# Optimization experiments

Hardware: AMD Instinct MI355X
Metric: run time of the kernel (lower is better)

The kernel has to match this reference:

```python
import jax, jax.numpy as jnp
import numpy as np
from jax import lax

B, C, H, W = 16, 256, 32, 32
HK, WK = 16, 16
NH = 8              # num_heads
HD = C // NH        # head_dim = 32
N = H * W           # 1024
M = HK * WK         # 256
EXP = 3             # attn_expansion
HID = NH * EXP      # 24 hidden channels in DLA
EPS = 1e-5


def setup_inputs() -> dict:
    key = jax.random.key(0)
    ks = jax.random.split(key, 16)
    s = 0.02
    return {
        "q": jax.random.normal(ks[0], (B, C, H, W), jnp.float32),
        "kv": jax.random.normal(ks[1], (B, C, HK, WK), jnp.float32),
        "Wq": jax.random.normal(ks[2], (C, C), jnp.float32) * s,
        "Wkv": jax.random.normal(ks[3], (2 * C, C), jnp.float32) * s,
        "Wp": jax.random.normal(ks[4], (C, C), jnp.float32) * s,
        "bp": jnp.zeros((C,), jnp.float32),
        "rpb": jnp.ones((N, M), jnp.float32),
        "W_exp": jax.random.normal(ks[5], (HID, NH), jnp.float32) * s,   # 1x1 conv heads->hidden
        "g1": jnp.ones((HID,), jnp.float32),
        "b1": jnp.zeros((HID,), jnp.float32),
        "W_dw": jax.random.normal(ks[6], (HID, 1, 3, 3), jnp.float32) * s,  # depthwise 3x3
        "g2": jnp.ones((HID,), jnp.float32),
        "b2": jnp.zeros((HID,), jnp.float32),
        "W_red": jax.random.normal(ks[7], (NH, HID), jnp.float32) * s,  # 1x1 conv hidden->heads
        "g3": jnp.ones((NH,), jnp.float32),
        "b3": jnp.zeros((NH,), jnp.float32),
    }


def group_norm(x, gamma, beta, groups):
    b, c, h, w = x.shape
    xg = x.reshape(b, groups, c // groups, h, w)
    mu = xg.mean(axis=(2, 3, 4), keepdims=True)
    var = xg.var(axis=(2, 3, 4), keepdims=True)
    xn = ((xg - mu) * lax.rsqrt(var + EPS)).reshape(b, c, h, w)
    return xn * gamma[None, :, None, None] + beta[None, :, None, None]


def swish(x):
    return x * jax.nn.sigmoid(x)


def dla(a, W_exp, g1, b1, W_dw, g2, b2, W_red, g3, b3):
    # a: [B, NH, N, M] treated as NCHW image with C=num_heads
    x = jnp.einsum('bcnm,oc->bonm', a, W_exp)              # 1x1 expand -> [B,HID,N,M]
    x = swish(group_norm(x, g1, b1, EXP))
    x = lax.conv_general_dilated(
        x, W_dw, window_strides=(1, 1), padding='SAME',
        feature_group_count=HID,
        dimension_numbers=('NCHW', 'OIHW', 'NCHW'))        # depthwise 3x3
    x = swish(group_norm(x, g2, b2, EXP))
    x = jnp.einsum('bcnm,oc->bonm', x, W_red)              # 1x1 reduce -> [B,NH,N,M]
    x = group_norm(x, g3, b3, 1)                            # no activation
    return x


def reference(q, kv, Wq, Wkv, Wp, bp, rpb, W_exp, g1, b1, W_dw, g2, b2, W_red, g3, b3):
    b = q.shape[0]
    scale = HD ** -0.5
    # kv path: [B,C,HK,WK] -> [B,M,C] -> Linear(C->2C)
    kv_t = kv.reshape(b, C, M).transpose(0, 2, 1)
    kvp = kv_t @ Wkv.T                                     # [B,M,2C]
    kvp = kvp.reshape(b, M, 2, NH, HD).transpose(2, 0, 3, 1, 4)  # [2,B,NH,M,HD]
    k, v = kvp[0], kvp[1]
    # q path: [B,C,H,W] -> [B,N,C] -> Linear -> [B,NH,N,HD]
    qf = (q.reshape(b, C, N).transpose(0, 2, 1) @ Wq.T)
    qh = qf.reshape(b, N, NH, HD).transpose(0, 2, 1, 3)
    attn = jnp.einsum('bhnd,bhmd->bhnm', qh, k) * scale + rpb[None, None]
    attn = jax.nn.softmax(attn, axis=-1)
    attn = dla(attn, W_exp, g1, b1, W_dw, g2, b2, W_red, g3, b3)
    out = jnp.einsum('bhnm,bhmd->bhnd', attn, v)           # [B,NH,N,HD]
    out = out.transpose(0, 2, 1, 3).reshape(b, N, C)
    out = out @ Wp.T + bp
    return out.transpose(0, 2, 1).reshape(b, C, H, W)
```

## Files before the change

### kernel.cpp

```cpp
#include <hip/hip_runtime.h>
#include <math.h>

#define Bb 16
#define Cc 256
#define Nn 1024
#define Mm 256
#define NHh 8
#define HDd 32
#define HIDh 24
#define NMs (Nn*Mm)
#define TTB 16
#define CHUNK 8
#define EPSf 1e-5f
#define SCALEf 0.17677669529663687f
#define STP 32

typedef float v2f __attribute__((ext_vector_type(2)));
typedef __attribute__((ext_vector_type(8))) short bf8v;
typedef __attribute__((ext_vector_type(4))) float f4v;

__device__ __forceinline__ float wave_sum(float v){
#pragma unroll
  for (int off=32; off; off>>=1) v += __shfl_xor(v, off, 64);
  return v;
}
__device__ __forceinline__ float sigm_(float x){ return __builtin_amdgcn_rcpf(1.f + __expf(-x)); }
__device__ __forceinline__ float swish_(float x){ return x * sigm_(x); }
__device__ __forceinline__ v2f swish2(v2f x){
  v2f r;
  r.x = x.x * sigm_(x.x);
  r.y = x.y * sigm_(x.y);
  return r;
}
__device__ __forceinline__ unsigned short f2bf(float f){
  unsigned u = __float_as_uint(f);
  u += 0x7fffu + ((u >> 16) & 1u);
  return (unsigned short)(u >> 16);
}
__device__ __forceinline__ unsigned cvtpk(float lo, float hi){
  unsigned r;
  asm("v_cvt_pk_bf16_f32 %0, %1, %2" : "=v"(r) : "v"(lo), "v"(hi));
  return r;
}
__device__ __forceinline__ float bfup(unsigned short s){ return __uint_as_float(((unsigned)s) << 16); }
__device__ __forceinline__ float bflo(unsigned u){ return __uint_as_float(u << 16); }
__device__ __forceinline__ float bfhi(unsigned u){ return __uint_as_float(u & 0xffff0000u); }
__device__ __forceinline__ void gload_lds16(const void* g, void* l){
  __builtin_amdgcn_global_load_lds(
      (const __attribute__((address_space(1))) unsigned int*)g,
      (__attribute__((address_space(3))) unsigned int*)l, 16, 0, 0);
}

template<int MODE>
__launch_bounds__(256)
__global__ void gemm_mfma(const float* __restrict__ A,
                          const float* __restrict__ W,
                          const float* __restrict__ bias,
                          float* __restrict__ O1, float* __restrict__ O2, int Isize)
{
  __shared__ __align__(16) unsigned short Wt[64 * 40];
  __shared__ __align__(16) unsigned short At[64 * 40];
  const int b = blockIdx.z;
  const int i0 = blockIdx.x * 64;
  const int j0 = blockIdx.y * 64;
  const int tid = threadIdx.x;
  const int lane = tid & 63, wv = tid >> 6;
  const int wj = (wv >> 1) * 32, wi = (wv & 1) * 32;
  const int l15 = lane & 15, l4 = lane >> 4;

  const float* Ab = A + (long)b * Cc * Isize;
  const int sj = tid >> 2, skh = (tid & 3) * 8;
  const int si = tid & 63, skb = (tid >> 6) * 8;

  f4v acc[2][2] = {};
  for (int k0 = 0; k0 < Cc; k0 += 32) {
    float wreg[8];
    {
      const float* wp = W + (long)(j0 + sj) * Cc + k0 + skh;
      *(f4v*)&wreg[0] = *(const f4v*)&wp[0];
      *(f4v*)&wreg[4] = *(const f4v*)&wp[4];
    }
    float areg[8];
    {
      const float* ap = Ab + (long)(k0 + skb) * Isize + i0 + si;
#pragma unroll
      for (int e = 0; e < 8; e++) areg[e] = ap[(long)e * Isize];
    }
    __syncthreads();
    {
      unsigned pk[4];
#pragma unroll
      for (int t = 0; t < 4; t++) pk[t] = cvtpk(wreg[2*t], wreg[2*t+1]);
      *(uint4*)&Wt[sj*40 + skh] = make_uint4(pk[0], pk[1], pk[2], pk[3]);
#pragma unroll
      for (int t = 0; t < 4; t++) pk[t] = cvtpk(areg[2*t], areg[2*t+1]);
      *(uint4*)&At[si*40 + skb] = make_uint4(pk[0], pk[1], pk[2], pk[3]);
    }
    __syncthreads();
    bf8v af[2], bf[2];
#pragma unroll
    for (int fm = 0; fm < 2; fm++)
      af[fm] = *(const bf8v*)&Wt[(wj + fm*16 + l15)*40 + l4*8];
#pragma unroll
    for (int fn = 0; fn < 2; fn++)
      bf[fn] = *(const bf8v*)&At[(wi + fn*16 + l15)*40 + l4*8];
#pragma unroll
    for (int fm = 0; fm < 2; fm++)
#pragma unroll
      for (int fn = 0; fn < 2; fn++)
        acc[fm][fn] = __builtin_amdgcn_mfma_f32_16x16x32_bf16(af[fm], bf[fn], acc[fm][fn], 0, 0, 0);
  }
#pragma unroll
  for (int fm = 0; fm < 2; fm++) {
    const int jb = j0 + wj + fm*16 + l4*4;
    f4v bv = {0.f, 0.f, 0.f, 0.f};
    if (MODE == 2) bv = *(const f4v*)&bias[jb];
#pragma unroll
    for (int fn = 0; fn < 2; fn++) {
      const int ii = i0 + wi + fn*16 + l15;
      if (MODE == 1) {
        const int two = jb >> 8, jj = jb & 255;
        const int h = jj >> 5, d0 = jj & 31;
        float* p = (two ? O2 : O1) + (((long)b * NHh + h) * Mm + ii) * HDd + d0;
#pragma unroll
        for (int r = 0; r < 4; r++) p[r] = acc[fm][fn][r];
      } else {
        float* op = O1 + ((long)b * Cc + jb) * (long)Isize + ii;
#pragma unroll
        for (int r = 0; r < 4; r++)
          op[(long)r * Isize] = acc[fm][fn][r] + bv[r];
      }
    }
  }
}

__launch_bounds__(256)
__global__ void compute_sv(const float* __restrict__ vb, float* __restrict__ sv)
{
  __shared__ float red[256];
  const int bh = blockIdx.x, tid = threadIdx.x;
  const int d = tid & 31, ch = tid >> 5;
  const float* vp = vb + (long)bh * Mm * HDd;
  float s = 0.f;
  for (int m = ch; m < Mm; m += 8) s += vp[m * HDd + d];
  red[tid] = s;
  __syncthreads();
  if (tid < 32) {
    float t = 0.f;
#pragma unroll
    for (int cc = 0; cc < 8; cc++) t += red[cc * 32 + tid];
    sv[(long)bh * HDd + tid] = t;
  }
}

__launch_bounds__(256)
__global__ void attn_softmax(const float* __restrict__ qhT, const float* __restrict__ kb,
                             const float* __restrict__ rpb, unsigned short* __restrict__ attn)
{
  __shared__ __align__(16) unsigned short Kt[Mm * 40];
  __shared__ __align__(16) unsigned short Qt[64 * 40];
  const int b = blockIdx.z, h = blockIdx.y, n0 = blockIdx.x * 64;
  const int tid = threadIdx.x;
  const int lane = tid & 63, wv = tid >> 6;
  const int l15 = lane & 15, l4 = lane >> 4;
  {
    const float* kp = kb + ((long)b * NHh + h) * Mm * HDd;
#pragma unroll
    for (int u = 0; u < 8; u++) {
      const int f = tid + u * 256;
      const int m = f >> 3, dq = (f & 7) * 4;
      const f4v k4 = *(const f4v*)&kp[m * HDd + dq];
      *(uint2*)&Kt[m * 40 + dq] = make_uint2(cvtpk(k4.x, k4.y), cvtpk(k4.z, k4.w));
    }
  }
  {
    const float* qp = qhT + ((long)b * NHh + h) * HDd * Nn + n0;
#pragma unroll
    for (int u = 0; u < 4; u++) {
      const int f = tid + u * 256;
      const int n = f & 63, d2 = (f >> 6) * 2;
      const float q0 = qp[(long)d2 * Nn + n];
      const float q1 = qp[(long)(d2 + 1) * Nn + n];
      *(unsigned*)&Qt[n * 40 + d2] = cvtpk(q0, q1);
    }
  }
  __syncthreads();
  const bf8v qf = *(const bf8v*)&Qt[(wv * 16 + l15) * 40 + l4 * 8];
  f4v S[16];
#pragma unroll
  for (int mt = 0; mt < 16; mt++) {
    const bf8v kf = *(const bf8v*)&Kt[(mt * 16 + l15) * 40 + l4 * 8];
    f4v z = {0.f, 0.f, 0.f, 0.f};
    S[mt] = __builtin_amdgcn_mfma_f32_16x16x32_bf16(kf, qf, z, 0, 0, 0);
  }
  const int n = n0 + wv * 16 + l15;
  const float* rp = rpb + (long)n * Mm;
  float mx = -1e30f;
#pragma unroll
  for (int mt = 0; mt < 16; mt++) {
    const f4v r4 = *(const f4v*)&rp[mt * 16 + l4 * 4];
    S[mt][0] = fmaf(S[mt][0], SCALEf, r4.x);
    S[mt][1] = fmaf(S[mt][1], SCALEf, r4.y);
    S[mt][2] = fmaf(S[mt][2], SCALEf, r4.z);
    S[mt][3] = fmaf(S[mt][3], SCALEf, r4.w);
    mx = fmaxf(mx, fmaxf(fmaxf(S[mt][0], S[mt][1]), fmaxf(S[mt][2], S[mt][3])));
  }
  mx = fmaxf(mx, __shfl_xor(mx, 16, 64));
  mx = fmaxf(mx, __shfl_xor(mx, 32, 64));
  float sum = 0.f;
#pragma unroll
  for (int mt = 0; mt < 16; mt++) {
    S[mt][0] = __expf(S[mt][0] - mx);
    S[mt][1] = __expf(S[mt][1] - mx);
    S[mt][2] = __expf(S[mt][2] - mx);
    S[mt][3] = __expf(S[mt][3] - mx);
    sum += (S[mt][0] + S[mt][1]) + (S[mt][2] + S[mt][3]);
  }
  sum += __shfl_xor(sum, 16, 64);
  sum += __shfl_xor(sum, 32, 64);
  const float inv = __builtin_amdgcn_rcpf(sum);
  unsigned short* ap = attn + (((long)b * NHh + h) * Nn + n) * Mm;
#pragma unroll
  for (int mt = 0; mt < 16; mt++) {
    const unsigned p0 = cvtpk(S[mt][0] * inv, S[mt][1] * inv);
    const unsigned p1 = cvtpk(S[mt][2] * inv, S[mt][3] * inv);
    *(uint2*)&ap[mt * 16 + l4 * 4] = make_uint2(p0, p1);
  }
}

__launch_bounds__(256)
__global__ void gram_stats(const unsigned short* __restrict__ attn, float* __restrict__ G)
{
  __shared__ float red[36][4];
  const int b = blockIdx.y, tid = threadIdx.x;
  const unsigned short* ap = attn + (long)b * NHh * NMs + (long)blockIdx.x * 2048 + tid * 8;
  float a[8][8];
#pragma unroll
  for (int h = 0; h < 8; h++) {
    const uint4 v = *(const uint4*)&ap[(long)h * NMs];
    a[h][0] = bflo(v.x); a[h][1] = bfhi(v.x); a[h][2] = bflo(v.y); a[h][3] = bfhi(v.y);
    a[h][4] = bflo(v.z); a[h][5] = bfhi(v.z); a[h][6] = bflo(v.w); a[h][7] = bfhi(v.w);
  }
  float g[36];
  int t = 0;
#pragma unroll
  for (int i = 0; i < 8; i++)
#pragma unroll
    for (int j = i; j < 8; j++, t++) {
      float s = 0.f;
#pragma unroll
      for (int m = 0; m < 8; m++) s = fmaf(a[i][m], a[j][m], s);
      g[t] = s;
    }
  const int lane = tid & 63, wid = tid >> 6;
#pragma unroll
  for (int t2 = 0; t2 < 36; t2++) {
    const float s = wave_sum(g[t2]);
    if (lane == 0) red[t2][wid] = s;
  }
  __syncthreads();
  if (tid < 36)
    atomicAdd(&G[((long)b * 36 + tid) * STP],
              red[tid][0] + red[tid][1] + red[tid][2] + red[tid][3]);
}

__launch_bounds__(768, 6)
__global__ void dla_pass_b(const unsigned short* __restrict__ attn,
                           const float* __restrict__ Wexp,
                           const float* __restrict__ g1, const float* __restrict__ b1,
                           const float* __restrict__ G, const float* __restrict__ Wdw,
                           unsigned short* __restrict__ x2, float* __restrict__ stats2c, int b0)
{
  __shared__ __align__(16) unsigned short sl[(TTB + 2) * NHh * Mm];
  const int tid = threadIdx.x;
  const int wv = tid >> 6, lane = tid & 63;
  const int bc = blockIdx.y, b = b0 + bc;
  const int n0 = blockIdx.x * TTB;
  const int c0 = wv * 2;
  const int g = wv >> 2;

  {
    const unsigned short* abase = attn + (long)b * NHh * NMs;
    const int q_lo = lane >> 5;
    const int m0 = (lane & 31) * 8;
#pragma unroll
    for (int i = 0; i < 6; i++) {
      const int pp = (wv * 6 + i) * 2;
      const int row = pp >> 3;
      const int nn = n0 - 1 + row;
      if (nn >= 0 && nn < Nn) {
        const int h = (pp + q_lo) & 7;
        gload_lds16(abase + (long)h * NMs + (long)nn * Mm + m0, &sl[pp * Mm]);
      }
    }
  }

  float mu, rs;
  {
    const float* Gb = G + (long)b * 36 * STP;
    float sum = 0.f, sumsq = 0.f;
    for (int c = g * 8; c < g * 8 + 8; c++) {
      float w[8];
#pragma unroll
      for (int h = 0; h < 8; h++) w[h] = Wexp[c * 8 + h];
      float wsu = 0.f;
#pragma unroll
      for (int h = 0; h < 8; h++) wsu += w[h];
      sum += wsu;
      float s2 = 0.f;
      int t = 0;
#pragma unroll
      for (int i = 0; i < 8; i++)
#pragma unroll
        for (int j = i; j < 8; j++, t++) {
          const float f = (i == j) ? 1.f : 2.f;
          s2 = fmaf(f * w[i] * w[j], Gb[t * STP], s2);
        }
      sumsq += s2;
    }
    const float cnt = 8.f * NMs;
    mu = sum * ((float)Nn / cnt);
    const float var = sumsq / cnt - mu * mu;
    rs = rsqrtf(var + EPSf);
  }
  v2f we2[8], wd2[9], B12;
  {
    const float A10 = rs * g1[c0], A11 = rs * g1[c0 + 1];
    B12.x = b1[c0] - mu * A10;
    B12.y = b1[c0 + 1] - mu * A11;
#pragma unroll
    for (int h = 0; h < NHh; h++) {
      we2[h].x = Wexp[c0 * NHh + h] * A10;
      we2[h].y = Wexp[(c0 + 1) * NHh + h] * A11;
    }
#pragma unroll
    for (int k = 0; k < 9; k++) {
      wd2[k].x = Wdw[c0 * 9 + k];
      wd2[k].y = Wdw[(c0 + 1) * 9 + k];
    }
  }
  __syncthreads();

  v2f s1p[4] = {}, s2p[4] = {};
  v2f smp = {0.f, 0.f}, sqp = {0.f, 0.f};
  for (int r = -1; r <= TTB; r++) {
    const int nn = n0 + r;
    const bool rowv = (nn >= 0 && nn < Nn);
    v2f xp[4];
    if (rowv) {
#pragma unroll
      for (int mi = 0; mi < 4; mi++) xp[mi] = B12;
      const unsigned short* sp = &sl[(r + 1) * NHh * Mm + lane * 4];
#pragma unroll
      for (int h = 0; h < NHh; h++) {
        const ushort4 v = *(const ushort4*)&sp[h * Mm];
        xp[0] += we2[h] * bfup(v.x);
        xp[1] += we2[h] * bfup(v.y);
        xp[2] += we2[h] * bfup(v.z);
        xp[3] += we2[h] * bfup(v.w);
      }
#pragma unroll
      for (int mi = 0; mi < 4; mi++) xp[mi] = swish2(xp[mi]);
    } else {
#pragma unroll
      for (int mi = 0; mi < 4; mi++) xp[mi] = (v2f){0.f, 0.f};
    }
    v2f xl, xr;
    xl.x = __shfl_up(xp[3].x, 1);  xl.y = __shfl_up(xp[3].y, 1);
    xr.x = __shfl_down(xp[0].x, 1); xr.y = __shfl_down(xp[0].y, 1);
    if (lane == 0)  { xl = (v2f){0.f, 0.f}; }
    if (lane == 63) { xr = (v2f){0.f, 0.f}; }
    const v2f L[4] = {xl, xp[0], xp[1], xp[2]};
    const v2f R[4] = {xp[1], xp[2], xp[3], xr};
    v2f y[4];
#pragma unroll
    for (int mi = 0; mi < 4; mi++) {
      const v2f u0 = wd2[0] * L[mi] + wd2[1] * xp[mi] + wd2[2] * R[mi];
      const v2f u1 = wd2[3] * L[mi] + wd2[4] * xp[mi] + wd2[5] * R[mi];
      const v2f u2 = wd2[6] * L[mi] + wd2[7] * xp[mi] + wd2[8] * R[mi];
      y[mi] = s2p[mi] + u2;
      s2p[mi] = s1p[mi] + u1;
      s1p[mi] = u0;
    }
    if (r >= 1) {
#pragma unroll
      for (int mi = 0; mi < 4; mi++) {
        smp += y[mi];
        sqp += y[mi] * y[mi];
      }
      const int nw = n0 + r - 1;
      const unsigned w0 = cvtpk(y[0].x, y[1].x), w1 = cvtpk(y[2].x, y[3].x);
      const unsigned w2 = cvtpk(y[0].y, y[1].y), w3 = cvtpk(y[2].y, y[3].y);
      unsigned short* xq = x2 + ((long)(bc * Nn + nw) * HIDh + c0) * Mm + lane * 4;
      *(uint2*)xq        = make_uint2(w0, w1);
      *(uint2*)(xq + Mm) = make_uint2(w2, w3);
    }
  }
  {
    const float vs0 = wave_sum(smp.x), vq0 = wave_sum(sqp.x);
    const float vs1 = wave_sum(smp.y), vq1 = wave_sum(sqp.y);
    if (lane == 0) {
      atomicAdd(&stats2c[((long)b * HIDh + c0) * STP], vs0);
      atomicAdd(&stats2c[((long)b * HIDh + c0) * STP + 1], vq0);
      atomicAdd(&stats2c[((long)b * HIDh + c0 + 1) * STP], vs1);
      atomicAdd(&stats2c[((long)b * HIDh + c0 + 1) * STP + 1], vq1);
    }
  }
}

__launch_bounds__(256)
__global__ void dla_pass_c(const unsigned short* __restrict__ x2, const float* __restrict__ g2,
                           const float* __restrict__ b2, const float* __restrict__ stats2c,
                           const float* __restrict__ Wred, unsigned short* __restrict__ a2,
                           float* __restrict__ partial3, int b0)
{
  __shared__ float wA[HIDh], wB[HIDh], wrs[HIDh][NHh];
  __shared__ float red2[2][4];
  const int tid = threadIdx.x;
  const int wv = tid >> 6, lane = tid & 63;
  const int bc = blockIdx.y, b = b0 + bc;
  if (tid < HIDh) {
    const int c = tid, g = c >> 3;
    float s = 0.f, q = 0.f;
#pragma unroll
    for (int cc = 0; cc < 8; cc++) {
      s += stats2c[((long)b * HIDh + g * 8 + cc) * STP];
      q += stats2c[((long)b * HIDh + g * 8 + cc) * STP + 1];
    }
    const float cnt = 8.f * NMs;
    const float mu = s / cnt;
    const float var = q / cnt - mu * mu;
    const float A2 = rsqrtf(var + EPSf) * g2[c];
    wA[c] = A2; wB[c] = b2[c] - mu * A2;
  }
  if (tid < HIDh * NHh) {
    const int c = tid >> 3, h = tid & 7;
    wrs[c][h] = Wred[h * HIDh + c];
  }
  __syncthreads();
  const int rsel = lane >> 5, ms = lane & 31;
  const int n = blockIdx.x * 8 + wv * 2 + rsel;
  const unsigned short* xp = x2 + (long)(bc * Nn + n) * HIDh * Mm + ms * 8;
  float red[NHh][8] = {};
#pragma unroll
  for (int c = 0; c < HIDh; c++) {
    const uint4 xv = *(const uint4*)&xp[c * Mm];
    const float Ac = wA[c], Bc = wB[c];
    float sw[8];
    sw[0] = swish_(fmaf(bflo(xv.x), Ac, Bc));
    sw[1] = swish_(fmaf(bfhi(xv.x), Ac, Bc));
    sw[2] = swish_(fmaf(bflo(xv.y), Ac, Bc));
    sw[3] = swish_(fmaf(bfhi(xv.y), Ac, Bc));
    sw[4] = swish_(fmaf(bflo(xv.z), Ac, Bc));
    sw[5] = swish_(fmaf(bfhi(xv.z), Ac, Bc));
    sw[6] = swish_(fmaf(bflo(xv.w), Ac, Bc));
    sw[7] = swish_(fmaf(bfhi(xv.w), Ac, Bc));
#pragma unroll
    for (int h = 0; h < NHh; h++) {
      const float w = wrs[c][h];
#pragma unroll
      for (int mi = 0; mi < 8; mi++) red[h][mi] = fmaf(w, sw[mi], red[h][mi]);
    }
  }
  float s3 = 0.f, q3 = 0.f;
#pragma unroll
  for (int h = 0; h < NHh; h++) {
    uint4 st;
    st.x = cvtpk(red[h][0], red[h][1]);
    st.y = cvtpk(red[h][2], red[h][3]);
    st.z = cvtpk(red[h][4], red[h][5]);
    st.w = cvtpk(red[h][6], red[h][7]);
    *(uint4*)&a2[(((long)b * NHh + h) * Nn + n) * Mm + ms * 8] = st;
#pragma unroll
    for (int mi = 0; mi < 8; mi++) {
      s3 += red[h][mi]; q3 = fmaf(red[h][mi], red[h][mi], q3);
    }
  }
  s3 = wave_sum(s3); q3 = wave_sum(q3);
  if (lane == 0) { red2[0][wv] = s3; red2[1][wv] = q3; }
  __syncthreads();
  if (tid < 2) {
    float t = red2[tid][0] + red2[tid][1] + red2[tid][2] + red2[tid][3];
    partial3[((long)b * 128 + blockIdx.x) * 2 + tid] = t;
  }
}

__launch_bounds__(128)
__global__ void finalize_stats3(const float* __restrict__ partial3, float* __restrict__ stats3)
{
  __shared__ float red2[2][2];
  const int b = blockIdx.x, tid = threadIdx.x;
  const int lane = tid & 63, wv = tid >> 6;
  float s = partial3[((long)b * 128 + tid) * 2];
  float q = partial3[((long)b * 128 + tid) * 2 + 1];
  s = wave_sum(s); q = wave_sum(q);
  if (lane == 0) { red2[0][wv] = s; red2[1][wv] = q; }
  __syncthreads();
  if (tid < 2)
    stats3[b * 2 + tid] = red2[tid][0] + red2[tid][1];
}

__launch_bounds__(256)
__global__ void pv_mfma(const unsigned short* __restrict__ a2, const float* __restrict__ vb,
                        const float* __restrict__ sv, const float* __restrict__ stats3,
                        const float* __restrict__ g3, const float* __restrict__ b3,
                        float* __restrict__ o)
{
  __shared__ __align__(16) unsigned short Vt[32 * 264];
  const int b = blockIdx.z, h = blockIdx.y, n0 = blockIdx.x * 128;
  const int tid = threadIdx.x;
  const int lane = tid & 63, wv = tid >> 6;
  const int l15 = lane & 15, l4 = lane >> 4;
  {
    const float* vp = vb + ((long)b * NHh + h) * Mm * HDd;
#pragma unroll
    for (int u = 0; u < 32; u++) {
      const int idx = tid + u * 256;
      const int m = idx >> 5, d = idx & 31;
      Vt[d * 264 + m] = f2bf(vp[idx]);
    }
  }
  __syncthreads();
  const unsigned short* ap = a2 + (((long)b * NHh + h) * Nn + n0) * Mm;
  f4v acc[2][2] = {};
#pragma unroll 2
  for (int k0 = 0; k0 < Mm; k0 += 32) {
    bf8v af[2], bf[2];
#pragma unroll
    for (int fm = 0; fm < 2; fm++)
      af[fm] = *(const bf8v*)&Vt[(fm * 16 + l15) * 264 + k0 + l4 * 8];
#pragma unroll
    for (int fn = 0; fn < 2; fn++)
      bf[fn] = *(const bf8v*)&ap[(long)(wv * 32 + fn * 16 + l15) * Mm + k0 + l4 * 8];
#pragma unroll
    for (int fm = 0; fm < 2; fm++)
#pragma unroll
      for (int fn = 0; fn < 2; fn++)
        acc[fm][fn] = __builtin_amdgcn_mfma_f32_16x16x32_bf16(af[fm], bf[fn], acc[fm][fn], 0, 0, 0);
  }
  const float cnt = (float)(NHh * NMs);
  const float mu = stats3[b * 2] / cnt;
  const float var = stats3[b * 2 + 1] / cnt - mu * mu;
  const float r3 = rsqrtf(var + EPSf);
  const float alpha = r3 * g3[h];
  const float beta = b3[h] - mu * alpha;
#pragma unroll
  for (int fm = 0; fm < 2; fm++) {
#pragma unroll
    for (int r = 0; r < 4; r++) {
      const int d = fm * 16 + l4 * 4 + r;
      const float bv = beta * sv[((long)b * NHh + h) * HDd + d];
      float* op = o + ((long)b * Cc + h * HDd + d) * Nn + n0 + wv * 32 + l15;
#pragma unroll
      for (int fn = 0; fn < 2; fn++)
        op[fn * 16] = fmaf(alpha, acc[fm][fn][r], bv);
    }
  }
}

extern "C" void kernel_launch(void* const* d_in, const int* in_sizes, int n_in,
                              void* d_out, int out_size, void* d_ws, size_t ws_size,
                              hipStream_t stream) {
  const float* q    = (const float*)d_in[0];
  const float* kv   = (const float*)d_in[1];
  const float* Wq   = (const float*)d_in[2];
  const float* Wkv  = (const float*)d_in[3];
  const float* Wp   = (const float*)d_in[4];
  const float* bp   = (const float*)d_in[5];
  const float* rpb  = (const float*)d_in[6];
  const float* Wexp = (const float*)d_in[7];
  const float* g1   = (const float*)d_in[8];
  const float* b1   = (const float*)d_in[9];
  const float* Wdw  = (const float*)d_in[10];
  const float* g2   = (const float*)d_in[11];
  const float* b2   = (const float*)d_in[12];
  const float* Wred = (const float*)d_in[13];
  const float* g3   = (const float*)d_in[14];
  const float* b3   = (const float*)d_in[15];
  float* out = (float*)d_out;

  float* ws = (float*)d_ws;
  size_t off = 0;
  auto alloc = [&](size_t n) { float* p = ws + off; off += n; return p; };
  float* attnf   = alloc((size_t)Bb * NHh * NMs / 2);
  float* a2f     = alloc((size_t)Bb * NHh * NMs / 2);
  float* big     = alloc((size_t)CHUNK * HIDh * NMs / 2);
  float* kbuf    = alloc((size_t)Bb * NHh * Mm * HDd);
  float* vbuf    = alloc((size_t)Bb * NHh * Mm * HDd);
  float* sv      = alloc((size_t)Bb * NHh * HDd);
  float* G       = alloc((size_t)Bb * 36 * STP);
  float* stats2c = alloc((size_t)Bb * HIDh * STP);
  float* stats3  = alloc(Bb * 2);
  float* partial3= alloc((size_t)Bb * 128 * 2);
  unsigned short* attn = (unsigned short*)attnf;
  unsigned short* a2 = (unsigned short*)a2f;
  float* qhT = big;
  unsigned short* x2 = (unsigned short*)big;
  float* oT = big;

  hipMemsetAsync(G, 0, (size_t)(Bb * 36 * STP + Bb * HIDh * STP) * sizeof(float), stream);

  gemm_mfma<0><<<dim3(Nn / 64, Cc / 64, Bb), 256, 0, stream>>>(q, Wq, nullptr, qhT, nullptr, Nn);
  gemm_mfma<1><<<dim3(Mm / 64, 512 / 64, Bb), 256, 0, stream>>>(kv, Wkv, nullptr, kbuf, vbuf, Mm);
  compute_sv<<<dim3(Bb * NHh), 256, 0, stream>>>(vbuf, sv);
  attn_softmax<<<dim3(Nn / 64, NHh, Bb), 256, 0, stream>>>(qhT, kbuf, rpb, attn);
  gram_stats<<<dim3(NMs / 2048, Bb), 256, 0, stream>>>(attn, G);

  for (int b0 = 0; b0 < Bb; b0 += CHUNK) {
    dla_pass_b<<<dim3(Nn / TTB, CHUNK), 768, 0, stream>>>(
        attn, Wexp, g1, b1, G, Wdw, x2, stats2c, b0);
    dla_pass_c<<<dim3(Nn / 8, CHUNK), 256, 0, stream>>>(
        x2, g2, b2, stats2c, Wred, a2, partial3, b0);
  }
  finalize_stats3<<<dim3(Bb), 128, 0, stream>>>(partial3, stats3);

  pv_mfma<<<dim3(Nn / 128, NHh, Bb), 256, 0, stream>>>(a2, vbuf, sv, stats3, g3, b3, oT);
  gemm_mfma<2><<<dim3(Nn / 64, Cc / 64, Bb), 256, 0, stream>>>(oT, Wp, bp, out, nullptr, Nn);
}
```

Baseline: 394.2 us.

## Store K/V as bf16, fuse sv and stats3 finalize into pv, pack dla_pass_c math

```diff
diff --git a/kernel.cpp b/kernel.cpp
--- a/kernel.cpp
+++ b/kernel.cpp
@@ -121,9 +121,10 @@
       if (MODE == 1) {
         const int two = jb >> 8, jj = jb & 255;
         const int h = jj >> 5, d0 = jj & 31;
-        float* p = (two ? O2 : O1) + (((long)b * NHh + h) * Mm + ii) * HDd + d0;
-#pragma unroll
-        for (int r = 0; r < 4; r++) p[r] = acc[fm][fn][r];
+        unsigned short* p = (unsigned short*)(two ? O2 : O1)
+                          + (((long)b * NHh + h) * Mm + ii) * HDd + d0;
+        *(uint2*)p = make_uint2(cvtpk(acc[fm][fn][0], acc[fm][fn][1]),
+                                cvtpk(acc[fm][fn][2], acc[fm][fn][3]));
       } else {
         float* op = O1 + ((long)b * Cc + jb) * (long)Isize + ii;
 #pragma unroll
@@ -135,26 +136,7 @@
 }
 
 __launch_bounds__(256)
-__global__ void compute_sv(const float* __restrict__ vb, float* __restrict__ sv)
-{
-  __shared__ float red[256];
-  const int bh = blockIdx.x, tid = threadIdx.x;
-  const int d = tid & 31, ch = tid >> 5;
-  const float* vp = vb + (long)bh * Mm * HDd;
-  float s = 0.f;
-  for (int m = ch; m < Mm; m += 8) s += vp[m * HDd + d];
-  red[tid] = s;
-  __syncthreads();
-  if (tid < 32) {
-    float t = 0.f;
-#pragma unroll
-    for (int cc = 0; cc < 8; cc++) t += red[cc * 32 + tid];
-    sv[(long)bh * HDd + tid] = t;
-  }
-}
-
-__launch_bounds__(256)
-__global__ void attn_softmax(const float* __restrict__ qhT, const float* __restrict__ kb,
+__global__ void attn_softmax(const float* __restrict__ qhT, const unsigned short* __restrict__ kb,
                              const float* __restrict__ rpb, unsigned short* __restrict__ attn)
 {
   __shared__ __align__(16) unsigned short Kt[Mm * 40];
@@ -164,13 +146,12 @@
   const int lane = tid & 63, wv = tid >> 6;
   const int l15 = lane & 15, l4 = lane >> 4;
   {
-    const float* kp = kb + ((long)b * NHh + h) * Mm * HDd;
-#pragma unroll
-    for (int u = 0; u < 8; u++) {
+    const unsigned short* kp = kb + ((long)b * NHh + h) * Mm * HDd;
+#pragma unroll
+    for (int u = 0; u < 4; u++) {
       const int f = tid + u * 256;
-      const int m = f >> 3, dq = (f & 7) * 4;
-      const f4v k4 = *(const f4v*)&kp[m * HDd + dq];
-      *(uint2*)&Kt[m * 40 + dq] = make_uint2(cvtpk(k4.x, k4.y), cvtpk(k4.z, k4.w));
+      const int m = f >> 2, q8 = (f & 3) * 8;
+      *(uint4*)&Kt[m * 40 + q8] = *(const uint4*)&kp[m * HDd + q8];
     }
   }
   {
@@ -415,7 +396,7 @@
                            float* __restrict__ partial3, int b0)
 {
   __shared__ float wA[HIDh], wB[HIDh], wrs[HIDh][NHh];
-  __shared__ float red2[2][4];
+  __shared__ float red2s[2][4];
   const int tid = threadIdx.x;
   const int wv = tid >> 6, lane = tid & 63;
   const int bc = blockIdx.y, b = b0 + bc;
@@ -441,86 +422,105 @@
   const int rsel = lane >> 5, ms = lane & 31;
   const int n = blockIdx.x * 8 + wv * 2 + rsel;
   const unsigned short* xp = x2 + (long)(bc * Nn + n) * HIDh * Mm + ms * 8;
-  float red[NHh][8] = {};
+  v2f red[NHh][4] = {};
 #pragma unroll
   for (int c = 0; c < HIDh; c++) {
     const uint4 xv = *(const uint4*)&xp[c * Mm];
-    const float Ac = wA[c], Bc = wB[c];
-    float sw[8];
-    sw[0] = swish_(fmaf(bflo(xv.x), Ac, Bc));
-    sw[1] = swish_(fmaf(bfhi(xv.x), Ac, Bc));
-    sw[2] = swish_(fmaf(bflo(xv.y), Ac, Bc));
-    sw[3] = swish_(fmaf(bfhi(xv.y), Ac, Bc));
-    sw[4] = swish_(fmaf(bflo(xv.z), Ac, Bc));
-    sw[5] = swish_(fmaf(bfhi(xv.z), Ac, Bc));
-    sw[6] = swish_(fmaf(bflo(xv.w), Ac, Bc));
-    sw[7] = swish_(fmaf(bfhi(xv.w), Ac, Bc));
+    const v2f A2 = {wA[c], wA[c]}, B2 = {wB[c], wB[c]};
+    v2f xw[4];
+    xw[0] = (v2f){bflo(xv.x), bfhi(xv.x)};
+    xw[1] = (v2f){bflo(xv.y), bfhi(xv.y)};
+    xw[2] = (v2f){bflo(xv.z), bfhi(xv.z)};
+    xw[3] = (v2f){bflo(xv.w), bfhi(xv.w)};
+#pragma unroll
+    for (int mi = 0; mi < 4; mi++) xw[mi] = swish2(xw[mi] * A2 + B2);
 #pragma unroll
     for (int h = 0; h < NHh; h++) {
       const float w = wrs[c][h];
-#pragma unroll
-      for (int mi = 0; mi < 8; mi++) red[h][mi] = fmaf(w, sw[mi], red[h][mi]);
-    }
-  }
-  float s3 = 0.f, q3 = 0.f;
+      const v2f w2 = {w, w};
+#pragma unroll
+      for (int mi = 0; mi < 4; mi++) red[h][mi] += w2 * xw[mi];
+    }
+  }
+  v2f s3v = {0.f, 0.f}, q3v = {0.f, 0.f};
 #pragma unroll
   for (int h = 0; h < NHh; h++) {
     uint4 st;
-    st.x = cvtpk(red[h][0], red[h][1]);
-    st.y = cvtpk(red[h][2], red[h][3]);
-    st.z = cvtpk(red[h][4], red[h][5]);
-    st.w = cvtpk(red[h][6], red[h][7]);
+    st.x = cvtpk(red[h][0].x, red[h][0].y);
+    st.y = cvtpk(red[h][1].x, red[h][1].y);
+    st.z = cvtpk(red[h][2].x, red[h][2].y);
+    st.w = cvtpk(red[h][3].x, red[h][3].y);
     *(uint4*)&a2[(((long)b * NHh + h) * Nn + n) * Mm + ms * 8] = st;
 #pragma unroll
-    for (int mi = 0; mi < 8; mi++) {
-      s3 += red[h][mi]; q3 = fmaf(red[h][mi], red[h][mi], q3);
-    }
-  }
+    for (int mi = 0; mi < 4; mi++) {
+      s3v += red[h][mi];
+      q3v += red[h][mi] * red[h][mi];
+    }
+  }
+  float s3 = s3v.x + s3v.y, q3 = q3v.x + q3v.y;
   s3 = wave_sum(s3); q3 = wave_sum(q3);
-  if (lane == 0) { red2[0][wv] = s3; red2[1][wv] = q3; }
+  if (lane == 0) { red2s[0][wv] = s3; red2s[1][wv] = q3; }
   __syncthreads();
   if (tid < 2) {
-    float t = red2[tid][0] + red2[tid][1] + red2[tid][2] + red2[tid][3];
+    float t = red2s[tid][0] + red2s[tid][1] + red2s[tid][2] + red2s[tid][3];
     partial3[((long)b * 128 + blockIdx.x) * 2 + tid] = t;
   }
 }
 
-__launch_bounds__(128)
-__global__ void finalize_stats3(const float* __restrict__ partial3, float* __restrict__ stats3)
-{
-  __shared__ float red2[2][2];
-  const int b = blockIdx.x, tid = threadIdx.x;
-  const int lane = tid & 63, wv = tid >> 6;
-  float s = partial3[((long)b * 128 + tid) * 2];
-  float q = partial3[((long)b * 128 + tid) * 2 + 1];
-  s = wave_sum(s); q = wave_sum(q);
-  if (lane == 0) { red2[0][wv] = s; red2[1][wv] = q; }
-  __syncthreads();
-  if (tid < 2)
-    stats3[b * 2 + tid] = red2[tid][0] + red2[tid][1];
-}
-
 __launch_bounds__(256)
-__global__ void pv_mfma(const unsigned short* __restrict__ a2, const float* __restrict__ vb,
-                        const float* __restrict__ sv, const float* __restrict__ stats3,
+__global__ void pv_mfma(const unsigned short* __restrict__ a2, const unsigned short* __restrict__ vb,
+                        const float* __restrict__ partial3,
                         const float* __restrict__ g3, const float* __restrict__ b3,
                         float* __restrict__ o)
 {
   __shared__ __align__(16) unsigned short Vt[32 * 264];
+  __shared__ float svl[32][9];
+  __shared__ float r4s[4];
   const int b = blockIdx.z, h = blockIdx.y, n0 = blockIdx.x * 128;
   const int tid = threadIdx.x;
   const int lane = tid & 63, wv = tid >> 6;
   const int l15 = lane & 15, l4 = lane >> 4;
   {
-    const float* vp = vb + ((long)b * NHh + h) * Mm * HDd;
+    const unsigned short* vp = vb + ((long)b * NHh + h) * Mm * HDd;
 #pragma unroll
     for (int u = 0; u < 32; u++) {
       const int idx = tid + u * 256;
       const int m = idx >> 5, d = idx & 31;
-      Vt[d * 264 + m] = f2bf(vp[idx]);
-    }
-  }
-  __syncthreads();
+      Vt[d * 264 + m] = vp[idx];
+    }
+  }
+  float pv_;
+  {
+    const int half = tid >> 7, i = tid & 127;
+    pv_ = partial3[((long)b * 128 + i) * 2 + half];
+  }
+  __syncthreads();
+  {
+    const int d = tid & 31, seg = tid >> 5;
+    float s = 0.f;
+#pragma unroll
+    for (int mm = 0; mm < 32; mm++) s += bfup(Vt[d * 264 + seg * 32 + mm]);
+    svl[d][seg] = s;
+  }
+  {
+    const float w = wave_sum(pv_);
+    if (lane == 0) r4s[wv] = w;
+  }
+  __syncthreads();
+  if (tid < 32) {
+    float t = 0.f;
+#pragma unroll
+    for (int seg = 0; seg < 8; seg++) t += svl[tid][seg];
+    svl[tid][0] = t;
+  }
+  __syncthreads();
+  const float cnt = (float)(NHh * NMs);
+  const float mu = (r4s[0] + r4s[1]) / cnt;
+  const float var = (r4s[2] + r4s[3]) / cnt - mu * mu;
+  const float r3 = rsqrtf(var + EPSf);
+  const float alpha = r3 * g3[h];
+  const float beta = b3[h] - mu * alpha;
+
   const unsigned short* ap = a2 + (((long)b * NHh + h) * Nn + n0) * Mm;
   f4v acc[2][2] = {};
 #pragma unroll 2
@@ -538,18 +538,12 @@
       for (int fn = 0; fn < 2; fn++)
         acc[fm][fn] = __builtin_amdgcn_mfma_f32_16x16x32_bf16(af[fm], bf[fn], acc[fm][fn], 0, 0, 0);
   }
-  const float cnt = (float)(NHh * NMs);
-  const float mu = stats3[b * 2] / cnt;
-  const float var = stats3[b * 2 + 1] / cnt - mu * mu;
-  const float r3 = rsqrtf(var + EPSf);
-  const float alpha = r3 * g3[h];
-  const float beta = b3[h] - mu * alpha;
 #pragma unroll
   for (int fm = 0; fm < 2; fm++) {
 #pragma unroll
     for (int r = 0; r < 4; r++) {
       const int d = fm * 16 + l4 * 4 + r;
-      const float bv = beta * sv[((long)b * NHh + h) * HDd + d];
+      const float bv = beta * svl[d][0];
       float* op = o + ((long)b * Cc + h * HDd + d) * Nn + n0 + wv * 32 + l15;
 #pragma unroll
       for (int fn = 0; fn < 2; fn++)
@@ -587,13 +581,13 @@
   float* big     = alloc((size_t)CHUNK * HIDh * NMs / 2);
   float* kbuf    = alloc((size_t)Bb * NHh * Mm * HDd);
   float* vbuf    = alloc((size_t)Bb * NHh * Mm * HDd);
-  float* sv      = alloc((size_t)Bb * NHh * HDd);
   float* G       = alloc((size_t)Bb * 36 * STP);
   float* stats2c = alloc((size_t)Bb * HIDh * STP);
-  float* stats3  = alloc(Bb * 2);
   float* partial3= alloc((size_t)Bb * 128 * 2);
   unsigned short* attn = (unsigned short*)attnf;
   unsigned short* a2 = (unsigned short*)a2f;
+  unsigned short* kb16 = (unsigned short*)kbuf;
+  unsigned short* vb16 = (unsigned short*)vbuf;
   float* qhT = big;
   unsigned short* x2 = (unsigned short*)big;
   float* oT = big;
@@ -602,8 +596,7 @@
 
   gemm_mfma<0><<<dim3(Nn / 64, Cc / 64, Bb), 256, 0, stream>>>(q, Wq, nullptr, qhT, nullptr, Nn);
   gemm_mfma<1><<<dim3(Mm / 64, 512 / 64, Bb), 256, 0, stream>>>(kv, Wkv, nullptr, kbuf, vbuf, Mm);
-  compute_sv<<<dim3(Bb * NHh), 256, 0, stream>>>(vbuf, sv);
-  attn_softmax<<<dim3(Nn / 64, NHh, Bb), 256, 0, stream>>>(qhT, kbuf, rpb, attn);
+  attn_softmax<<<dim3(Nn / 64, NHh, Bb), 256, 0, stream>>>(qhT, kb16, rpb, attn);
   gram_stats<<<dim3(NMs / 2048, Bb), 256, 0, stream>>>(attn, G);
 
   for (int b0 = 0; b0 < Bb; b0 += CHUNK) {
@@ -612,8 +605,7 @@
     dla_pass_c<<<dim3(Nn / 8, CHUNK), 256, 0, stream>>>(
         x2, g2, b2, stats2c, Wred, a2, partial3, b0);
   }
-  finalize_stats3<<<dim3(Bb), 128, 0, stream>>>(partial3, stats3);
-
-  pv_mfma<<<dim3(Nn / 128, NHh, Bb), 256, 0, stream>>>(a2, vbuf, sv, stats3, g3, b3, oT);
+
+  pv_mfma<<<dim3(Nn / 128, NHh, Bb), 256, 0, stream>>>(a2, vb16, partial3, g3, b3, oT);
   gemm_mfma<2><<<dim3(Nn / 64, Cc / 64, Bb), 256, 0, stream>>>(oT, Wp, bp, out, nullptr, Nn);
 }
```

After: 371.8 us. -5.7%, faster.
